# Performance work log

Measured on AMD Instinct MI355X. Metric: run time of the kernel, lower is better.

Reference implementation:

```python
import jax, jax.numpy as jnp
import numpy as np

DIM = 1024
HEADS = 16
SEQ_H = 32
SEQ_W = 32
HEAD_DIM = DIM // HEADS          # 64
ROT_DIM = HEAD_DIM // 4          # 16 per axis (lucidrains RotaryEmbedding dim)
FULL_ROT = 2 * ROT_DIM           # 32 channels rotated (axial: H-axis + W-axis)


def axial_freqs():
    # lucidrains 'pixel' mode: freqs = linspace(1, max_freq/2, dim//2) * pi, pos = linspace(-1, 1, steps)
    max_freq = SEQ_H * SEQ_W
    base = jnp.linspace(1.0, max_freq / 2.0, ROT_DIM // 2) * jnp.pi  # (rot//2,)
    th = jnp.linspace(-1.0, 1.0, SEQ_H)[:, None] * base[None, :]     # (H, rot//2)
    tw = jnp.linspace(-1.0, 1.0, SEQ_W)[:, None] * base[None, :]     # (W, rot//2)
    fh = jnp.repeat(th, 2, axis=-1)                                   # (H, rot)
    fw = jnpp_repeat = jnp.repeat(tw, 2, axis=-1)                     # (W, rot)
    fh = jnp.broadcast_to(fh[:, None, :], (SEQ_H, SEQ_W, ROT_DIM))
    fw = jnp.broadcast_to(fw[None, :, :], (SEQ_H, SEQ_W, ROT_DIM))
    return jnp.concatenate([fh, fw], axis=-1)                         # (H, W, FULL_ROT)


def rotate_half(t):
    # '... (d r) -> ... d r' with r=2, then (-x2, x1) interleaved back
    x = t.reshape(t.shape[:-1] + (t.shape[-1] // 2, 2))
    x1, x2 = x[..., 0], x[..., 1]
    return jnp.stack([-x2, x1], axis=-1).reshape(t.shape)


def apply_rope(t, cos, sin):
    # t: (B, heads, H, W, head_dim); only first FULL_ROT channels are rotated
    t_rot, t_pass = t[..., :FULL_ROT], t[..., FULL_ROT:]
    t_rot = t_rot * cos + rotate_half(t_rot) * sin
    return jnp.concatenate([t_rot, t_pass], axis=-1)


def setup_inputs() -> dict:
    key = jax.random.key(0)
    k1, k2, k3 = jax.random.split(key, 3)
    B, N = 8, SEQ_H * SEQ_W
    x = jax.random.normal(k1, (B, N, DIM), dtype=jnp.float32)
    Wqkv = jax.random.normal(k2, (3 * DIM, DIM), dtype=jnp.float32) * 0.02
    Wproj = jax.random.normal(k3, (DIM, DIM), dtype=jnp.float32) * 0.02
    bproj = jnp.zeros((DIM,), dtype=jnp.float32)
    return {"x": x, "Wqkv": Wqkv, "Wproj": Wproj, "bproj": bproj}


def reference(x, Wqkv, Wproj, bproj):
    B, N, C = x.shape
    qkv = jnp.einsum('bnc,fc->bnf', x, Wqkv)          # (B, N, 3C)
    q, k, v = jnp.split(qkv, 3, axis=-1)

    def to_grid(t):  # (B, N, C) -> (B, heads, H, W, hd)
        return t.reshape(B, SEQ_H, SEQ_W, HEADS, HEAD_DIM).transpose(0, 3, 1, 2, 4)

    q, k, v = to_grid(q), to_grid(k), to_grid(v)
    freqs = axial_freqs()
    cos, sin = jnp.cos(freqs), jnp.sin(freqs)         # (H, W, FULL_ROT)
    q = apply_rope(q, cos, sin)
    k = apply_rope(k, cos, sin)

    q = q.reshape(B, HEADS, N, HEAD_DIM)
    k = k.reshape(B, HEADS, N, HEAD_DIM)
    v = v.reshape(B, HEADS, N, HEAD_DIM)

    scale = 1.0 / jnp.sqrt(jnp.float32(HEAD_DIM))
    scores = jnp.einsum('bhqd,bhkd->bhqk', q, k) * scale
    attn = jax.nn.softmax(scores, axis=-1)
    out = jnp.einsum('bhqk,bhkd->bhqd', attn, v)       # (B, heads, N, hd)
    out = out.transpose(0, 2, 1, 3).reshape(B, N, C)
    return jnp.einsum('bnc,oc->bno', out, Wproj) + bproj
```

## Files before the change

kernel.cpp:

```cpp
#include <hip/hip_runtime.h>
#include <math.h>

#define DIM_ 1024
#define HEADS_ 16
#define HD_ 64
#define B_ 8
#define N_ 1024
#define M_TOT 8192

typedef __attribute__((ext_vector_type(4))) float f32x4;
typedef _Float16 v8h __attribute__((ext_vector_type(8)));
typedef __attribute__((ext_vector_type(4))) unsigned int u32x4;

static __device__ __forceinline__ unsigned short f2h(float x) {
  _Float16 h = (_Float16)x;
  return __builtin_bit_cast(unsigned short, h);
}
static __device__ __forceinline__ float fexp2(float x) {
  return __builtin_amdgcn_exp2f(x);
}
static __device__ __forceinline__ unsigned pkh2(float a, float b) {
  auto t = __builtin_amdgcn_cvt_pkrtz(a, b);
  return __builtin_bit_cast(unsigned, t);
}

static __device__ __forceinline__ void gload16(unsigned short* lds_base,
                                               const unsigned short* g) {
  __builtin_amdgcn_global_load_lds(
      (const __attribute__((address_space(1))) unsigned int*)g,
      (__attribute__((address_space(3))) unsigned int*)lds_base, 16, 0, 0);
}

__global__ __launch_bounds__(256) void split_all_k(
    const float* __restrict__ x, const float* __restrict__ wqkv,
    const float* __restrict__ wproj,
    unsigned short* __restrict__ xh, unsigned short* __restrict__ wqh,
    unsigned short* __restrict__ wph) {
  const int i = blockIdx.x * 256 + threadIdx.x;
  const float4* src;
  unsigned short* dst;
  int j;
  if (i < 2097152)      { j = i;           src = (const float4*)x;     dst = xh;  }
  else if (i < 2883584) { j = i - 2097152; src = (const float4*)wqkv;  dst = wqh; }
  else                  { j = i - 2883584; src = (const float4*)wproj; dst = wph; }
  float4 v = src[j];
  ushort4 h;
  h.x = f2h(v.x); h.y = f2h(v.y); h.z = f2h(v.z); h.w = f2h(v.w);
  ((ushort4*)dst)[j] = h;
}

__global__ void rope_table_k(float* cs, float* sn) {
  int i = threadIdx.x;
  if (i < 256) {
    int pos = i >> 3, j = i & 7;
    double u = -1.0 + (double)pos * (2.0/31.0);
    double ang = u * ((1.0 + 73.0*(double)j) * 3.14159265358979323846);
    cs[i] = (float)cos(ang);
    sn[i] = (float)sin(ang);
  }
}

static __device__ __forceinline__ void gemm_core1(
    const unsigned short* __restrict__ ah, const unsigned short* __restrict__ bh,
    unsigned short* S0, unsigned short* S2,
    int m0, int f0, f32x4 acc[4][4]) {
  const int tid = threadIdx.x;
  const int w = tid >> 6, l = tid & 63;
  const int lg = l >> 4, lc = l & 15;
  const int wr = w >> 1, wc = w & 1;
  const int r8 = l >> 3;
  const int ch = (l & 7) ^ r8;
  const int kc = ch * 8;
  for (int k0 = 0; k0 < 1024; k0 += 64) {
#pragma unroll
    for (int r = 0; r < 4; ++r) {
      const int row = r*32 + w*8 + r8;
      const size_t ao = (size_t)(m0 + row)*1024 + k0 + kc;
      const size_t bo = (size_t)(f0 + row)*1024 + k0 + kc;
      const int d = r*2048 + w*512;
      gload16(S0 + d, ah + ao);
      gload16(S2 + d, bh + bo);
    }
    __syncthreads();
#pragma unroll
    for (int c = 0; c < 2; ++c) {
      v8h a0[4], b0[4];
#pragma unroll
      for (int mi = 0; mi < 4; ++mi) {
        const int row = wr*64 + mi*16 + lc;
        const int bo = row*128 + ((c*64 + lg*16) ^ ((row & 7) << 4));
        a0[mi] = *(const v8h*)((const char*)S0 + bo);
      }
#pragma unroll
      for (int nj = 0; nj < 4; ++nj) {
        const int row = wc*64 + nj*16 + lc;
        const int bo = row*128 + ((c*64 + lg*16) ^ ((row & 7) << 4));
        b0[nj] = *(const v8h*)((const char*)S2 + bo);
      }
#pragma unroll
      for (int mi = 0; mi < 4; ++mi)
#pragma unroll
        for (int nj = 0; nj < 4; ++nj)
          acc[mi][nj] = __builtin_amdgcn_mfma_f32_16x16x32_f16(a0[mi], b0[nj], acc[mi][nj], 0, 0, 0);
    }
    __syncthreads();
  }
}

__global__ __launch_bounds__(256) void qk_gemm_mfma(
    const unsigned short* __restrict__ xh,
    const unsigned short* __restrict__ wh,
    const float* __restrict__ cs, const float* __restrict__ sn,
    unsigned short* __restrict__ qh, unsigned short* __restrict__ kh) {
  __shared__ unsigned short SM[16384];
  const int tid = threadIdx.x;
  const int w = tid >> 6, l = tid & 63;
  const int lg = l >> 4, lc = l & 15;
  const int wr = w >> 1, wc = w & 1;
  const int nwg = gridDim.x * gridDim.y;
  int bid = blockIdx.y * gridDim.x + blockIdx.x;
  bid = (bid & 7) * (nwg >> 3) + (bid >> 3);
  const int m0 = (bid / gridDim.x) * 128;
  const int f0 = (bid % gridDim.x) * 128;
  f32x4 acc[4][4] = {};
  gemm_core1(xh, wh, SM, SM + 8192, m0, f0, acc);
  const int qsel = f0 >> 10;
  const int head = ((f0 & 1023) >> 6) + wc;
  float* tbl = (float*)SM;
  tbl[tid] = cs[tid];
  tbl[256 + tid] = sn[tid];
  __syncthreads();
  const float scale = (qsel == 0) ? 0.18033688011112042f : 1.0f;
  unsigned short* oh = qsel ? kh : qh;
#pragma unroll
  for (int mi = 0; mi < 4; ++mi)
#pragma unroll
    for (int nj = 0; nj < 4; ++nj) {
      const int d = nj*16 + lc;
#pragma unroll
      for (int r = 0; r < 4; ++r) {
        const int m = m0 + wr*64 + mi*16 + lg*4 + r;
        const int b = m >> 10, n = m & 1023;
        float val = acc[mi][nj][r] * scale;
        float part = __shfl_xor(val, 1);
        if (nj < 2) {
          const int p = d >> 1;
          const int pos = (p < 8) ? (n >> 5) : (n & 31);
          const float c = tbl[pos*8 + (p & 7)];
          const float s = tbl[256 + pos*8 + (p & 7)];
          val = (d & 1) ? (val*c + part*s) : (val*c - part*s);
        }
        oh[((size_t)(b*HEADS_ + head)*N_ + n)*HD_ + d] = f2h(val);
      }
    }
}

__global__ __launch_bounds__(256) void v_gemm_mfma(
    const unsigned short* __restrict__ xh, const unsigned short* __restrict__ wh,
    unsigned short* __restrict__ vth) {
  __shared__ unsigned short SM[18432];
  const int tid = threadIdx.x;
  const int w = tid >> 6, l = tid & 63;
  const int lg = l >> 4, lc = l & 15;
  const int wr = w >> 1, wc = w & 1;
  const int nwg = gridDim.x * gridDim.y;
  int bid = blockIdx.y * gridDim.x + blockIdx.x;
  bid = (bid & 7) * (nwg >> 3) + (bid >> 3);
  const int m0 = (bid / gridDim.x) * 128;
  const int f0 = (bid % gridDim.x) * 128;
  f32x4 acc[4][4] = {};
  gemm_core1(xh, wh + (size_t)2048*1024, SM, SM + 8192, m0, f0, acc);
  __syncthreads();
  unsigned short* VT = SM + w * 4608;
#pragma unroll
  for (int mi = 0; mi < 4; ++mi)
#pragma unroll
    for (int nj = 0; nj < 4; ++nj)
#pragma unroll
      for (int r = 0; r < 4; r += 2) {
        const int ml = mi*16 + lg*4 + r;
        const int dl = nj*16 + lc;
        *(unsigned*)((char*)VT + dl*144 + ml*2) = pkh2(acc[mi][nj][r], acc[mi][nj][r+1]);
      }
  __syncthreads();
  const int b = m0 >> 10;
  const int n0 = (m0 & 1023) + wr*64;
  const int head = (f0 >> 6) + wc;
#pragma unroll
  for (int j = 0; j < 8; ++j) {
    const int dl = (l >> 3) + j*8;
    u32x4 val = *(const u32x4*)((const char*)VT + dl*144 + (l & 7)*16);
    *(u32x4*)(vth + ((size_t)((b*HEADS_ + head)*HD_ + dl))*N_ + n0 + (l & 7)*8) = val;
  }
}

__global__ __launch_bounds__(256) void proj_gemm_mfma(
    const unsigned short* __restrict__ ah,
    const unsigned short* __restrict__ wh,
    const float* __restrict__ bias, float* __restrict__ out) {
  __shared__ unsigned short SM[16384];
  const int tid = threadIdx.x;
  const int w = tid >> 6, l = tid & 63;
  const int lg = l >> 4, lc = l & 15;
  const int wr = w >> 1, wc = w & 1;
  const int nwg = gridDim.x * gridDim.y;
  int bid = blockIdx.y * gridDim.x + blockIdx.x;
  bid = (bid & 7) * (nwg >> 3) + (bid >> 3);
  const int m0 = (bid / gridDim.x) * 128;
  const int o0 = (bid % gridDim.x) * 128;
  f32x4 acc[4][4] = {};
  gemm_core1(ah, wh, SM, SM + 8192, m0, o0, acc);
#pragma unroll
  for (int nj = 0; nj < 4; ++nj) {
    const int o = o0 + wc*64 + nj*16 + lc;
    const float bv = bias[o];
#pragma unroll
    for (int mi = 0; mi < 4; ++mi)
#pragma unroll
      for (int r = 0; r < 4; ++r) {
        const int m = m0 + wr*64 + mi*16 + lg*4 + r;
        out[(size_t)m*DIM_ + o] = acc[mi][nj][r] + bv;
      }
  }
}

__global__ __launch_bounds__(256, 8) void attn_mfma_k(
    const unsigned short* __restrict__ qh,
    const unsigned short* __restrict__ kh,
    const unsigned short* __restrict__ vth,
    unsigned short* __restrict__ aoh) {
  __shared__ unsigned short KhS[4096];
  __shared__ unsigned short VhS[4096];
  const int tid = threadIdx.x;
  const int w = tid >> 6, l = tid & 63;
  const int lg = l >> 4, lc = l & 15;
  const int bh = blockIdx.x, qt = blockIdx.y;
  const size_t gb = (size_t)bh * (N_*HD_);

  v8h qf[2];
#pragma unroll
  for (int c = 0; c < 2; ++c)
    qf[c] = *(const v8h*)(qh + gb +
        (size_t)(qt*64 + w*16 + lc)*HD_ + c*32 + lg*8);
  f32x4 O[4];
#pragma unroll
  for (int dt = 0; dt < 4; ++dt) O[dt] = (f32x4){0.f, 0.f, 0.f, 0.f};
  float lrow = 0.f;

  const int sr8 = l >> 3;
  const int sch = (l & 7) ^ sr8;
  const int sig0 = (w >> 1)*32 + (sr8 >> 2)*8 + (w & 1)*4 + (sr8 & 3);

  for (int t = 0; t < 16; ++t) {
#pragma unroll
    for (int i = 0; i < 2; ++i) {
      const int lb = (w*16 + i*8)*64;
      gload16(KhS + lb, kh + gb + (size_t)(t*64 + sig0 + i*16)*HD_ + sch*8);
      gload16(VhS + lb, vth + gb + (size_t)(w*16 + i*8 + sr8)*N_ + t*64 + sch*8);
    }
    __syncthreads();
    f32x4 s[4];
    __builtin_amdgcn_s_setprio(1);
#pragma unroll
    for (int kt = 0; kt < 4; ++kt) {
      s[kt] = (f32x4){0.f, 0.f, 0.f, 0.f};
      const int row = kt*16 + lc;
      const int sw = (row & 7) << 4;
#pragma unroll
      for (int c = 0; c < 2; ++c) {
        v8h kf = *(const v8h*)((const char*)KhS + row*128 + ((c*64 + lg*16) ^ sw));
        s[kt] = __builtin_amdgcn_mfma_f32_16x16x32_f16(kf, qf[c], s[kt], 0, 0, 0);
      }
    }
    __builtin_amdgcn_s_setprio(0);
    u32x4 pa[2];
#pragma unroll
    for (int c = 0; c < 2; ++c) {
      const float p0 = fexp2(s[2*c][0]);
      const float p1 = fexp2(s[2*c][1]);
      const float p2 = fexp2(s[2*c][2]);
      const float p3 = fexp2(s[2*c][3]);
      const float p4 = fexp2(s[2*c+1][0]);
      const float p5 = fexp2(s[2*c+1][1]);
      const float p6 = fexp2(s[2*c+1][2]);
      const float p7 = fexp2(s[2*c+1][3]);
      lrow += ((p0 + p1) + (p2 + p3)) + ((p4 + p5) + (p6 + p7));
      pa[c] = (u32x4){pkh2(p0, p1), pkh2(p2, p3), pkh2(p4, p5), pkh2(p6, p7)};
    }
    __builtin_amdgcn_s_setprio(1);
#pragma unroll
    for (int dt = 0; dt < 4; ++dt) {
      const int row = dt*16 + lc;
      const int sw = (row & 7) << 4;
#pragma unroll
      for (int c = 0; c < 2; ++c) {
        v8h vf = *(const v8h*)((const char*)VhS + row*128 + ((c*64 + lg*16) ^ sw));
        O[dt] = __builtin_amdgcn_mfma_f32_16x16x32_f16(
            __builtin_bit_cast(v8h, pa[c]), vf, O[dt], 0, 0, 0);
      }
    }
    __builtin_amdgcn_s_setprio(0);
    __syncthreads();
  }
  lrow += __shfl_xor(lrow, 16);
  lrow += __shfl_xor(lrow, 32);
  const int b = bh >> 4, h = bh & 15;
  const float myinv = 1.0f / lrow;
#pragma unroll
  for (int r = 0; r < 4; ++r) {
    const float iv = __shfl(myinv, lg*4 + r);
    const int n = qt*64 + w*16 + lg*4 + r;
    const size_t base = ((size_t)(b*N_ + n))*DIM_ + h*HD_ + lc;
#pragma unroll
    for (int dt = 0; dt < 4; ++dt)
      aoh[base + dt*16] = f2h(O[dt][r] * iv);
  }
}

extern "C" void kernel_launch(void* const* d_in, const int* in_sizes, int n_in,
                              void* d_out, int out_size, void* d_ws, size_t ws_size,
                              hipStream_t stream) {
  const float* x     = (const float*)d_in[0];
  const float* Wqkv  = (const float*)d_in[1];
  const float* Wproj = (const float*)d_in[2];
  const float* bproj = (const float*)d_in[3];
  float* out = (float*)d_out;

  unsigned short* xh  = (unsigned short*)d_ws;
  unsigned short* wqh = xh  + 8388608;
  unsigned short* wph = wqh + 3145728;
  unsigned short* qh  = wph + 1048576;
  unsigned short* kh  = qh  + 8388608;
  unsigned short* vth = kh  + 8388608;
  float* cs = (float*)(vth + 8388608);
  float* sn = cs + 256;
  unsigned short* aoh = xh;

  hipLaunchKernelGGL(rope_table_k, dim3(1), dim3(256), 0, stream, cs, sn);
  hipLaunchKernelGGL(split_all_k, dim3(12288), dim3(256), 0, stream,
                     x, Wqkv, Wproj, xh, wqh, wph);
  hipLaunchKernelGGL(qk_gemm_mfma, dim3(16, 64), dim3(256), 0, stream,
                     xh, wqh, cs, sn, qh, kh);
  hipLaunchKernelGGL(v_gemm_mfma, dim3(8, 64), dim3(256), 0, stream, xh, wqh, vth);
  hipLaunchKernelGGL(attn_mfma_k, dim3(128, 16), dim3(256), 0, stream,
                     qh, kh, vth, aoh);
  hipLaunchKernelGGL(proj_gemm_mfma, dim3(8, 64), dim3(256), 0, stream,
                     aoh, wph, bproj, out);
}
```

Measured before the change: 168.6 us.

## Double-buffer GEMM K-loop with 32-wide tiles and widen attention key tiles to 128

The shared GEMM core now uses a two-stage shared-memory ping-pong with K-step 32, so the next tile's global-to-LDS loads are issued before the current tile's MFMAs. This removes one barrier per iteration, adds MFMA priority hints, and swizzles the 64-byte row layout. The attention kernel stages 128 keys per iteration instead of 64, halving loop trips and barriers. In exchange it doubles that kernel's LDS use and lowers its occupancy hint from 8 to 5 blocks.

Result: faster. 161.6 us (-4.2%).

```diff
diff --git a/kernel.cpp b/kernel.cpp
--- a/kernel.cpp
+++ b/kernel.cpp
@@ -60,49 +60,58 @@
   }
 }
 
-static __device__ __forceinline__ void gemm_core1(
+static __device__ __forceinline__ void gemm_core2ph(
     const unsigned short* __restrict__ ah, const unsigned short* __restrict__ bh,
-    unsigned short* S0, unsigned short* S2,
+    unsigned short* SM,
     int m0, int f0, f32x4 acc[4][4]) {
   const int tid = threadIdx.x;
   const int w = tid >> 6, l = tid & 63;
   const int lg = l >> 4, lc = l & 15;
   const int wr = w >> 1, wc = w & 1;
-  const int r8 = l >> 3;
-  const int ch = (l & 7) ^ r8;
-  const int kc = ch * 8;
-  for (int k0 = 0; k0 < 1024; k0 += 64) {
-#pragma unroll
-    for (int r = 0; r < 4; ++r) {
-      const int row = r*32 + w*8 + r8;
-      const size_t ao = (size_t)(m0 + row)*1024 + k0 + kc;
-      const size_t bo = (size_t)(f0 + row)*1024 + k0 + kc;
-      const int d = r*2048 + w*512;
-      gload16(S0 + d, ah + ao);
-      gload16(S2 + d, bh + bo);
-    }
-    __syncthreads();
-#pragma unroll
-    for (int c = 0; c < 2; ++c) {
-      v8h a0[4], b0[4];
-#pragma unroll
-      for (int mi = 0; mi < 4; ++mi) {
-        const int row = wr*64 + mi*16 + lc;
-        const int bo = row*128 + ((c*64 + lg*16) ^ ((row & 7) << 4));
-        a0[mi] = *(const v8h*)((const char*)S0 + bo);
-      }
-#pragma unroll
-      for (int nj = 0; nj < 4; ++nj) {
-        const int row = wc*64 + nj*16 + lc;
-        const int bo = row*128 + ((c*64 + lg*16) ^ ((row & 7) << 4));
-        b0[nj] = *(const v8h*)((const char*)S2 + bo);
-      }
-#pragma unroll
-      for (int mi = 0; mi < 4; ++mi)
-#pragma unroll
-        for (int nj = 0; nj < 4; ++nj)
-          acc[mi][nj] = __builtin_amdgcn_mfma_f32_16x16x32_f16(a0[mi], b0[nj], acc[mi][nj], 0, 0, 0);
-    }
+  const int r64 = tid >> 2;
+  const int ch  = tid & 3;
+  const int wof = w * 512;
+  const unsigned short* A = ah + (size_t)m0 * 1024;
+  const unsigned short* B = bh + (size_t)f0 * 1024;
+
+  auto stg = [&](const unsigned short* base, int t, unsigned short* dst) {
+#pragma unroll
+    for (int i = 0; i < 2; ++i) {
+      const int row = i*64 + r64;
+      const int sc = ch ^ ((row >> 1) & 3);
+      gload16(dst + i*2048 + wof, base + (size_t)row*1024 + t*32 + sc*8);
+    }
+  };
+
+  stg(A, 0, SM);
+  stg(B, 0, SM + 4096);
+  __syncthreads();
+#pragma unroll 2
+  for (int t = 0; t < 32; ++t) {
+    unsigned short* cur = SM + (t & 1) * 8192;
+    unsigned short* nxt = SM + ((t & 1) ^ 1) * 8192;
+    if (t < 31) {
+      stg(A, t + 1, nxt);
+      stg(B, t + 1, nxt + 4096);
+    }
+    v8h a0[4], b0[4];
+#pragma unroll
+    for (int mi = 0; mi < 4; ++mi) {
+      const int row = wr*64 + mi*16 + lc;
+      a0[mi] = *(const v8h*)((const char*)cur + row*64 + ((lg ^ ((row >> 1) & 3)) << 4));
+    }
+#pragma unroll
+    for (int nj = 0; nj < 4; ++nj) {
+      const int row = wc*64 + nj*16 + lc;
+      b0[nj] = *(const v8h*)((const char*)(cur + 4096) + row*64 + ((lg ^ ((row >> 1) & 3)) << 4));
+    }
+    __builtin_amdgcn_s_setprio(1);
+#pragma unroll
+    for (int mi = 0; mi < 4; ++mi)
+#pragma unroll
+      for (int nj = 0; nj < 4; ++nj)
+        acc[mi][nj] = __builtin_amdgcn_mfma_f32_16x16x32_f16(a0[mi], b0[nj], acc[mi][nj], 0, 0, 0);
+    __builtin_amdgcn_s_setprio(0);
     __syncthreads();
   }
 }
@@ -123,7 +132,7 @@
   const int m0 = (bid / gridDim.x) * 128;
   const int f0 = (bid % gridDim.x) * 128;
   f32x4 acc[4][4] = {};
-  gemm_core1(xh, wh, SM, SM + 8192, m0, f0, acc);
+  gemm_core2ph(xh, wh, SM, m0, f0, acc);
   const int qsel = f0 >> 10;
   const int head = ((f0 & 1023) >> 6) + wc;
   float* tbl = (float*)SM;
@@ -169,7 +178,7 @@
   const int m0 = (bid / gridDim.x) * 128;
   const int f0 = (bid % gridDim.x) * 128;
   f32x4 acc[4][4] = {};
-  gemm_core1(xh, wh + (size_t)2048*1024, SM, SM + 8192, m0, f0, acc);
+  gemm_core2ph(xh, wh + (size_t)2048*1024, SM, m0, f0, acc);
   __syncthreads();
   unsigned short* VT = SM + w * 4608;
 #pragma unroll
@@ -209,7 +218,7 @@
   const int m0 = (bid / gridDim.x) * 128;
   const int o0 = (bid % gridDim.x) * 128;
   f32x4 acc[4][4] = {};
-  gemm_core1(ah, wh, SM, SM + 8192, m0, o0, acc);
+  gemm_core2ph(ah, wh, SM, m0, o0, acc);
 #pragma unroll
   for (int nj = 0; nj < 4; ++nj) {
     const int o = o0 + wc*64 + nj*16 + lc;
@@ -224,13 +233,13 @@
   }
 }
 
-__global__ __launch_bounds__(256, 8) void attn_mfma_k(
+__global__ __launch_bounds__(256, 5) void attn_mfma_k(
     const unsigned short* __restrict__ qh,
     const unsigned short* __restrict__ kh,
     const unsigned short* __restrict__ vth,
     unsigned short* __restrict__ aoh) {
-  __shared__ unsigned short KhS[4096];
-  __shared__ unsigned short VhS[4096];
+  __shared__ unsigned short KhS[8192];
+  __shared__ unsigned short VhS[8192];
   const int tid = threadIdx.x;
   const int w = tid >> 6, l = tid & 63;
   const int lg = l >> 4, lc = l & 15;
@@ -247,59 +256,68 @@
   for (int dt = 0; dt < 4; ++dt) O[dt] = (f32x4){0.f, 0.f, 0.f, 0.f};
   float lrow = 0.f;
 
-  const int sr8 = l >> 3;
-  const int sch = (l & 7) ^ sr8;
-  const int sig0 = (w >> 1)*32 + (sr8 >> 2)*8 + (w & 1)*4 + (sr8 & 3);
-
-  for (int t = 0; t < 16; ++t) {
-#pragma unroll
-    for (int i = 0; i < 2; ++i) {
-      const int lb = (w*16 + i*8)*64;
-      gload16(KhS + lb, kh + gb + (size_t)(t*64 + sig0 + i*16)*HD_ + sch*8);
-      gload16(VhS + lb, vth + gb + (size_t)(w*16 + i*8 + sr8)*N_ + t*64 + sch*8);
+  const int wof = w * 512;
+  const int kpr = tid >> 3;
+  const int ksc = (tid & 7) ^ (kpr & 7);
+  const int vr  = tid >> 4;
+  const int vsc = (tid & 15) ^ (vr & 15);
+
+  for (int t = 0; t < 8; ++t) {
+#pragma unroll
+    for (int i = 0; i < 4; ++i) {
+      const int p = i*32 + kpr;
+      const int kap = ((p >> 5) << 5) | (((p >> 2) & 3) << 3)
+                    | (((p >> 4) & 1) << 2) | (p & 3);
+      gload16(KhS + i*2048 + wof, kh + gb + (size_t)(t*128 + kap)*HD_ + ksc*8);
+      const int row = i*16 + vr;
+      gload16(VhS + i*2048 + wof, vth + gb + (size_t)row*N_ + t*128 + vsc*8);
     }
     __syncthreads();
-    f32x4 s[4];
-    __builtin_amdgcn_s_setprio(1);
-#pragma unroll
-    for (int kt = 0; kt < 4; ++kt) {
-      s[kt] = (f32x4){0.f, 0.f, 0.f, 0.f};
-      const int row = kt*16 + lc;
-      const int sw = (row & 7) << 4;
-#pragma unroll
-      for (int c = 0; c < 2; ++c) {
-        v8h kf = *(const v8h*)((const char*)KhS + row*128 + ((c*64 + lg*16) ^ sw));
-        s[kt] = __builtin_amdgcn_mfma_f32_16x16x32_f16(kf, qf[c], s[kt], 0, 0, 0);
-      }
-    }
-    __builtin_amdgcn_s_setprio(0);
-    u32x4 pa[2];
-#pragma unroll
-    for (int c = 0; c < 2; ++c) {
-      const float p0 = fexp2(s[2*c][0]);
-      const float p1 = fexp2(s[2*c][1]);
-      const float p2 = fexp2(s[2*c][2]);
-      const float p3 = fexp2(s[2*c][3]);
-      const float p4 = fexp2(s[2*c+1][0]);
-      const float p5 = fexp2(s[2*c+1][1]);
-      const float p6 = fexp2(s[2*c+1][2]);
-      const float p7 = fexp2(s[2*c+1][3]);
-      lrow += ((p0 + p1) + (p2 + p3)) + ((p4 + p5) + (p6 + p7));
-      pa[c] = (u32x4){pkh2(p0, p1), pkh2(p2, p3), pkh2(p4, p5), pkh2(p6, p7)};
-    }
-    __builtin_amdgcn_s_setprio(1);
-#pragma unroll
-    for (int dt = 0; dt < 4; ++dt) {
-      const int row = dt*16 + lc;
-      const int sw = (row & 7) << 4;
-#pragma unroll
-      for (int c = 0; c < 2; ++c) {
-        v8h vf = *(const v8h*)((const char*)VhS + row*128 + ((c*64 + lg*16) ^ sw));
-        O[dt] = __builtin_amdgcn_mfma_f32_16x16x32_f16(
-            __builtin_bit_cast(v8h, pa[c]), vf, O[dt], 0, 0, 0);
-      }
-    }
-    __builtin_amdgcn_s_setprio(0);
+#pragma unroll
+    for (int h = 0; h < 2; ++h) {
+      f32x4 s[4];
+      __builtin_amdgcn_s_setprio(1);
+#pragma unroll
+      for (int k4 = 0; k4 < 4; ++k4) {
+        s[k4] = (f32x4){0.f, 0.f, 0.f, 0.f};
+        const int row = (h*4 + k4)*16 + lc;
+        const int sw = (row & 7) << 4;
+#pragma unroll
+        for (int c = 0; c < 2; ++c) {
+          v8h kf = *(const v8h*)((const char*)KhS + row*128 + ((c*64 + lg*16) ^ sw));
+          s[k4] = __builtin_amdgcn_mfma_f32_16x16x32_f16(kf, qf[c], s[k4], 0, 0, 0);
+        }
+      }
+      __builtin_amdgcn_s_setprio(0);
+      u32x4 pa[2];
+#pragma unroll
+      for (int cc = 0; cc < 2; ++cc) {
+        const float p0 = fexp2(s[2*cc][0]);
+        const float p1 = fexp2(s[2*cc][1]);
+        const float p2 = fexp2(s[2*cc][2]);
+        const float p3 = fexp2(s[2*cc][3]);
+        const float p4 = fexp2(s[2*cc+1][0]);
+        const float p5 = fexp2(s[2*cc+1][1]);
+        const float p6 = fexp2(s[2*cc+1][2]);
+        const float p7 = fexp2(s[2*cc+1][3]);
+        lrow += ((p0 + p1) + (p2 + p3)) + ((p4 + p5) + (p6 + p7));
+        pa[cc] = (u32x4){pkh2(p0, p1), pkh2(p2, p3), pkh2(p4, p5), pkh2(p6, p7)};
+      }
+      __builtin_amdgcn_s_setprio(1);
+#pragma unroll
+      for (int dt = 0; dt < 4; ++dt) {
+        const int row = dt*16 + lc;
+        const int sw = (row & 15) << 4;
+#pragma unroll
+        for (int cc = 0; cc < 2; ++cc) {
+          const int c = h*2 + cc;
+          v8h vf = *(const v8h*)((const char*)VhS + row*256 + ((c*64 + lg*16) ^ sw));
+          O[dt] = __builtin_amdgcn_mfma_f32_16x16x32_f16(
+              __builtin_bit_cast(v8h, pa[cc]), vf, O[dt], 0, 0, 0);
+        }
+      }
+      __builtin_amdgcn_s_setprio(0);
+    }
     __syncthreads();
   }
   lrow += __shfl_xor(lrow, 16);
```
